# Kernel optimization log

Measured on AMD Instinct MI355X. Metric: run time of the kernel, lower is better.

The kernel has to match this reference:

```python
import jax, jax.numpy as jnp
import numpy as np

T, HID, H, KV, D = 2048, 2048, 16, 8, 128
EPS = 1e-6
THETA = 10000.0


def setup_inputs() -> dict:
    key = jax.random.key(0)
    ks = jax.random.split(key, 6)
    positions = jnp.arange(T, dtype=jnp.int64 if jax.config.jax_enable_x64 else jnp.int32)
    hidden_states = jax.random.normal(ks[0], (T, HID), dtype=jnp.float32)
    scale = 0.02
    Wq = jax.random.normal(ks[1], (HID, H * 2 * D), dtype=jnp.float32) * scale
    Wk = jax.random.normal(ks[2], (HID, KV * D), dtype=jnp.float32) * scale
    Wv = jax.random.normal(ks[3], (HID, KV * D), dtype=jnp.float32) * scale
    Wo = jax.random.normal(ks[4], (H * D, HID), dtype=jnp.float32) * scale
    q_norm_w = jnp.zeros((D,), dtype=jnp.float32)  # torch init: zeros, applied as (1+w)
    k_norm_w = jnp.zeros((D,), dtype=jnp.float32)
    return {"positions": positions, "hidden_states": hidden_states, "Wq": Wq,
            "Wk": Wk, "Wv": Wv, "Wo": Wo, "q_norm_w": q_norm_w, "k_norm_w": k_norm_w}


def _rms_norm(x, w):
    # fp32 RMSNorm with (1 + weight) scaling, per last dim
    xf = x.astype(jnp.float32)
    inv = jax.lax.rsqrt(jnp.mean(xf * xf, axis=-1, keepdims=True) + EPS)
    return (xf * inv * (1.0 + w.astype(jnp.float32))).astype(x.dtype)


def _rope(x, positions):
    # neox-style rotary over full head_dim; x: (T, heads, D)
    half = D // 2
    inv_freq = 1.0 / (THETA ** (jnp.arange(0, half, dtype=jnp.float32) / half))
    freqs = positions.astype(jnp.float32)[:, None] * inv_freq  # (T, half)
    cos = jnp.cos(freqs)[:, None, :]  # (T,1,half)
    sin = jnp.sin(freqs)[:, None, :]
    x1, x2 = x[..., :half], x[..., half:]
    return jnp.concatenate([x1 * cos - x2 * sin, x2 * cos + x1 * sin], axis=-1)


def reference(positions, hidden_states, Wq, Wk, Wv, Wo, q_norm_w, k_norm_w):
    scaling = D ** -0.5
    qg = (hidden_states @ Wq).reshape(T, H, 2 * D)
    q, gate = qg[..., :D], qg[..., D:]              # (T,H,D) each
    k = (hidden_states @ Wk).reshape(T, KV, D)
    v = (hidden_states @ Wv).reshape(T, KV, D)
    q = _rms_norm(q, q_norm_w)
    k = _rms_norm(k, k_norm_w)
    q = _rope(q, positions)
    k = _rope(k, positions)
    # GQA: repeat kv heads
    rep = H // KV
    k = jnp.repeat(k, rep, axis=1)                   # (T,H,D)
    v = jnp.repeat(v, rep, axis=1)
    scores = jnp.einsum('thd,shd->hts', q, k) * scaling  # (H,T,T)
    causal = positions[:, None] >= positions[None, :]     # (T,T)
    scores = jnp.where(causal[None], scores, jnp.finfo(scores.dtype).min)
    probs = jax.nn.softmax(scores, axis=-1)
    o = jnp.einsum('hts,shd->thd', probs, v).reshape(T, H * D)
    o = o * jax.nn.sigmoid(gate.reshape(T, H * D))
    return o @ Wo
```

## Files before the change

kernel.cpp:

```cpp
#include <hip/hip_runtime.h>
#include <stdint.h>
#include <math.h>

#define T_SEQ 2048
#define HID   2048
#define NH    16
#define NKV   8
#define DH    128

typedef __bf16 bf16x8 __attribute__((ext_vector_type(8)));
typedef float  f32x4  __attribute__((ext_vector_type(4)));

__device__ __forceinline__ ushort f2bf(float f) {
  uint32_t u = __float_as_uint(f);
  u += 0x7FFF + ((u >> 16) & 1);
  return (ushort)(u >> 16);
}
__device__ __forceinline__ ushort f2bf_rz(float f) {
  return (ushort)(__float_as_uint(f) >> 16);
}
__device__ __forceinline__ float bf2f(ushort u) {
  return __uint_as_float(((uint32_t)u) << 16);
}
__device__ __forceinline__ void gld16(const void* g, void* l) {
  __builtin_amdgcn_global_load_lds(
      (const __attribute__((address_space(1))) uint32_t*)g,
      (__attribute__((address_space(3))) uint32_t*)l, 16, 0, 0);
}

__global__ __launch_bounds__(256) void prep_kernel(
    const float* __restrict__ hs, const float* __restrict__ Wq,
    const float* __restrict__ Wk, const float* __restrict__ Wv,
    const float* __restrict__ Wo, ushort* __restrict__ hs16,
    ushort* __restrict__ Wqt, ushort* __restrict__ Wkt,
    ushort* __restrict__ Wvt, ushort* __restrict__ Wot) {
  int bid = blockIdx.x;
  if (bid < 4096) {
    int i = (bid * 256 + threadIdx.x) * 4;
    float4 v = *(const float4*)(hs + i);
    ushort4 o = {f2bf(v.x), f2bf(v.y), f2bf(v.z), f2bf(v.w)};
    *(ushort4*)(hs16 + i) = o;
    return;
  }
  bid -= 4096;
  const float* src; ushort* dst; int N, bi, bj;
  if (bid < 2048)      { src = Wq; dst = Wqt; N = 4096; bj = bid & 63; bi = bid >> 6; }
  else if (bid < 2560) { bid -= 2048; src = Wk; dst = Wkt; N = 1024; bj = bid & 15; bi = bid >> 4; }
  else if (bid < 3072) { bid -= 2560; src = Wv; dst = Wvt; N = 1024; bj = bid & 15; bi = bid >> 4; }
  else                 { bid -= 3072; src = Wo; dst = Wot; N = 2048; bj = bid & 31; bi = bid >> 5; }
  __shared__ float tile[64][65];
  const int r = threadIdx.x >> 2, cg = (threadIdx.x & 3) * 16;
  const float* sp = src + (size_t)(bi * 64 + r) * N + bj * 64 + cg;
#pragma unroll
  for (int p = 0; p < 4; ++p) {
    float4 v = *(const float4*)(sp + p * 4);
    tile[r][cg + p * 4 + 0] = v.x; tile[r][cg + p * 4 + 1] = v.y;
    tile[r][cg + p * 4 + 2] = v.z; tile[r][cg + p * 4 + 3] = v.w;
  }
  __syncthreads();
  ushort* dp = dst + (size_t)(bj * 64 + r) * HID + bi * 64 + cg;
#pragma unroll
  for (int p = 0; p < 2; ++p) {
    union { uint4 v; ushort u[8]; } o;
#pragma unroll
    for (int j = 0; j < 8; ++j) o.u[j] = f2bf(tile[cg + p * 8 + j][r]);
    *(uint4*)(dp + p * 8) = o.v;
  }
}

template <int MI>
__device__ __forceinline__ void gemm_loop(
    const ushort* __restrict__ A, const ushort* __restrict__ Bt,
    int K, int m0, int n0, ushort* As, ushort* Bs, f32x4 (*acc)[4]) {
  const int tid = threadIdx.x, lane = tid & 63, w = tid >> 6;
  const int quad = lane >> 4, l15 = lane & 15;
  const int wm = (w >> 1) * (MI * 16), wn = (w & 1) * 64;
  const int srow = tid >> 2, sch = tid & 3;
  for (int k0 = 0; k0 < K; k0 += 32) {
    __syncthreads();
#pragma unroll
    for (int p = 0; p < MI / 2; ++p) {
      int row = p * 64 + srow;
      int gch = sch ^ ((row >> 1) & 3);
      gld16(A + (size_t)(m0 + row) * K + k0 + gch * 8,
            As + (p * 256 + w * 64) * 8);
    }
#pragma unroll
    for (int p = 0; p < 2; ++p) {
      int row = p * 64 + srow;
      int gch = sch ^ ((row >> 1) & 3);
      gld16(Bt + (size_t)(n0 + row) * K + k0 + gch * 8,
            Bs + (p * 256 + w * 64) * 8);
    }
    __syncthreads();
    bf16x8 af[MI], bfr[4];
#pragma unroll
    for (int mi = 0; mi < MI; ++mi) {
      int row = wm + mi * 16 + l15;
      int pch = quad ^ ((row >> 1) & 3);
      af[mi] = *(const bf16x8*)(As + row * 32 + pch * 8);
    }
#pragma unroll
    for (int ni = 0; ni < 4; ++ni) {
      int row = wn + ni * 16 + l15;
      int pch = quad ^ ((row >> 1) & 3);
      bfr[ni] = *(const bf16x8*)(Bs + row * 32 + pch * 8);
    }
#pragma unroll
    for (int mi = 0; mi < MI; ++mi)
#pragma unroll
      for (int ni = 0; ni < 4; ++ni)
        acc[mi][ni] = __builtin_amdgcn_mfma_f32_16x16x32_bf16(
            af[mi], bfr[ni], acc[mi][ni], 0, 0, 0);
  }
}

__device__ __forceinline__ void bf16_store(f32x4 (*acc)[4],
                                           ushort* __restrict__ Cb, int Ncols,
                                           int m0, int n0) {
  const int lane = threadIdx.x & 63, w = threadIdx.x >> 6;
  const int quad = lane >> 4, l15 = lane & 15;
  const int wm = (w >> 1) * 64, wn = (w & 1) * 64;
#pragma unroll
  for (int mi = 0; mi < 4; ++mi)
#pragma unroll
    for (int ni = 0; ni < 4; ++ni)
#pragma unroll
      for (int r = 0; r < 4; ++r) {
        int row = m0 + wm + mi * 16 + quad * 4 + r;
        int col = n0 + wn + ni * 16 + l15;
        Cb[(size_t)row * Ncols + col] = f2bf(acc[mi][ni][r]);
      }
}

__global__ __launch_bounds__(256) void gemm_qkv(
    const ushort* __restrict__ hs16, const ushort* __restrict__ Wqt,
    const ushort* __restrict__ Wkt, const ushort* __restrict__ Wvt,
    ushort* __restrict__ q16, ushort* __restrict__ gate16,
    ushort* __restrict__ k16, ushort* __restrict__ v16t) {
  __shared__ ushort As[128 * 32];
  __shared__ ushort Bs[128 * 32];
  f32x4 acc[4][4];
#pragma unroll
  for (int i = 0; i < 4; ++i)
#pragma unroll
    for (int j = 0; j < 4; ++j) acc[i][j] = (f32x4){0.f, 0.f, 0.f, 0.f};
  const int b = blockIdx.x;
  if (b < 512) {
    int mt = b >> 5, nt = b & 31, m0 = mt * 128;
    gemm_loop<4>(hs16, Wqt, HID, m0, nt * 128, As, Bs, acc);
    ushort* dst = ((nt & 1) == 0) ? q16 : gate16;
    bf16_store(acc, dst, NH * DH, m0, (nt >> 1) * 128);
  } else if (b < 640) {
    int f = b - 512, m0 = (f >> 3) * 128, n0 = (f & 7) * 128;
    gemm_loop<4>(hs16, Wkt, HID, m0, n0, As, Bs, acc);
    bf16_store(acc, k16, 1024, m0, n0);
  } else {
    int f = b - 640, m0 = (f >> 4) * 128, n0 = (f & 15) * 128;
    gemm_loop<4>(Wvt, hs16, HID, m0, n0, As, Bs, acc);
    bf16_store(acc, v16t, T_SEQ, m0, n0);
  }
}

__global__ __launch_bounds__(256) void gemm_out(
    const ushort* __restrict__ ob16, const ushort* __restrict__ Wot,
    float* __restrict__ out) {
  __shared__ ushort As[64 * 32];
  __shared__ ushort Bs[128 * 32];
  f32x4 acc[2][4];
#pragma unroll
  for (int i = 0; i < 2; ++i)
#pragma unroll
    for (int j = 0; j < 4; ++j) acc[i][j] = (f32x4){0.f, 0.f, 0.f, 0.f};
  const int b = blockIdx.x;
  const int m0 = (b >> 4) * 64, n0 = (b & 15) * 128;
  gemm_loop<2>(ob16, Wot, HID, m0, n0, As, Bs, acc);
  const int lane = threadIdx.x & 63, w = threadIdx.x >> 6;
  const int quad = lane >> 4, l15 = lane & 15;
  const int wm = (w >> 1) * 32, wn = (w & 1) * 64;
#pragma unroll
  for (int mi = 0; mi < 2; ++mi)
#pragma unroll
    for (int ni = 0; ni < 4; ++ni)
#pragma unroll
      for (int r = 0; r < 4; ++r) {
        int row = m0 + wm + mi * 16 + quad * 4 + r;
        int col = n0 + wn + ni * 16 + l15;
        out[(size_t)row * HID + col] = acc[mi][ni][r];
      }
}

__global__ __launch_bounds__(128) void norm_qk(
    ushort* __restrict__ q16, ushort* __restrict__ k16,
    const int* __restrict__ positions, const float* __restrict__ qw,
    const float* __restrict__ kw) {
  const int t = blockIdx.x, hh = blockIdx.y, d = threadIdx.x;
  ushort* x; const float* wgt;
  if (hh < NH) { x = q16 + ((size_t)t * NH + hh) * DH; wgt = qw; }
  else         { x = k16 + ((size_t)t * NKV + (hh - NH)) * DH; wgt = kw; }
  float v = bf2f(x[d]);
  float ss = v * v;
#pragma unroll
  for (int off = 32; off >= 1; off >>= 1) ss += __shfl_xor(ss, off, 64);
  __shared__ float red[2];
  if ((d & 63) == 0) red[d >> 6] = ss;
  __syncthreads();
  float mean = (red[0] + red[1]) * (1.0f / 128.0f);
  float xn = v * rsqrtf(mean + 1e-6f) * (1.0f + wgt[d]);
  __shared__ float sh[128];
  sh[d] = xn;
  __syncthreads();
  if (d < 64) {
    float pos = (float)positions[t];
    float rev = pos * exp2f((float)d * -0.20762050593045233f) *
                0.15915494309189535f;
    float fr = rev - floorf(rev);
    float s = __builtin_amdgcn_sinf(fr);
    float c = __builtin_amdgcn_cosf(fr);
    float x1 = sh[d], x2 = sh[d + 64];
    x[d]      = f2bf(x1 * c - x2 * s);
    x[d + 64] = f2bf(x2 * c + x1 * s);
  }
}

__global__ __launch_bounds__(256) void attn_mfma(
    const ushort* __restrict__ q16, const ushort* __restrict__ k16,
    const ushort* __restrict__ v16t, const float* __restrict__ qnw,
    const float* __restrict__ knw, ushort* __restrict__ Op0,
    ushort* __restrict__ Op1, ushort* __restrict__ Op2,
    float* __restrict__ lpart) {
  const int pb = blockIdx.x, h = blockIdx.y, s = blockIdx.z, kvh = h >> 1;
  const int tid = threadIdx.x, lane = tid & 63, w = tid >> 6;
  const int quad = lane >> 4, l15 = lane & 15;

  __shared__ ushort Ks[64 * 128];
  __shared__ ushort Vs[144 * 64];
  __shared__ ushort Ps[4][16][72];

  for (int i = tid; i < 16 * 64; i += 256) {
    int row = 128 + (i >> 6), col = i & 63;
    Vs[row * 64 + col] = (row == 128) ? (ushort)0x3F80 : (ushort)0;
  }

  __shared__ float s8[8];
  __shared__ float bshare;
  {
    float mq = 0.f, mk = 0.f;
    if (tid < 128) { mq = fabsf(1.f + qnw[tid]); mk = fabsf(1.f + knw[tid]); }
#pragma unroll
    for (int off = 32; off >= 1; off >>= 1) {
      mq = fmaxf(mq, __shfl_xor(mq, off, 64));
      mk = fmaxf(mk, __shfl_xor(mk, off, 64));
    }
    if (lane == 0) { s8[w * 2] = mq; s8[w * 2 + 1] = mk; }
    __syncthreads();
    if (tid == 0) {
      float MQ = fmaxf(s8[0], s8[2]), MK = fmaxf(s8[1], s8[3]);
      bshare = 16.3217f * MQ * MK * 1.02f + 0.1f;
    }
    __syncthreads();
  }
  const float B = bshare;
  const float CSC = 0.08838834764831845f * 1.44269504088896f;

#pragma unroll 1
  for (int sel = 0; sel < 2; ++sel) {
    const int qt = sel ? (31 - pb) : pb;
    const int q0 = qt * 64;
    const int ntl = (qt >= s) ? ((qt - s) / 3 + 1) : 0;

    bf16x8 qf[4];
    const ushort* qbase = q16 + ((size_t)(q0 + w * 16 + l15) * NH + h) * DH;
#pragma unroll
    for (int ks = 0; ks < 4; ++ks)
      qf[ks] = *(const bf16x8*)(qbase + ks * 32 + quad * 8);

    f32x4 oacc[9];
#pragma unroll
    for (int i = 0; i < 9; ++i) oacc[i] = (f32x4){0.f, 0.f, 0.f, 0.f};

#pragma unroll 1
    for (int it = 0; it < ntl; ++it) {
      const int kt = s + 3 * it;
      const int kt0 = kt * 64;
      __syncthreads();
#pragma unroll
      for (int p = 0; p < 4; ++p) {
        int row = p * 16 + (tid >> 4), ch = tid & 15;
        int gch = ch ^ (row & 15);
        gld16(k16 + ((size_t)(kt0 + row) * NKV + kvh) * DH + gch * 8,
              Ks + (p * 256 + w * 64) * 8);
      }
#pragma unroll
      for (int p = 0; p < 4; ++p) {
        int row = p * 32 + (tid >> 3), ch = tid & 7;
        int gch = ch ^ (row & 7);
        gld16(v16t + (size_t)(kvh * DH + row) * T_SEQ + kt0 + gch * 8,
              Vs + (p * 256 + w * 64) * 8);
      }
      __syncthreads();

      f32x4 sacc[4];
#pragma unroll
      for (int ni = 0; ni < 4; ++ni) sacc[ni] = (f32x4){0.f, 0.f, 0.f, 0.f};
#pragma unroll
      for (int ks = 0; ks < 4; ++ks)
#pragma unroll
        for (int ni = 0; ni < 4; ++ni) {
          int row = ni * 16 + l15;
          int pch = (ks * 4 + quad) ^ (row & 15);
          bf16x8 kf = *(const bf16x8*)(Ks + row * 128 + pch * 8);
          sacc[ni] = __builtin_amdgcn_mfma_f32_16x16x32_bf16(
              qf[ks], kf, sacc[ni], 0, 0, 0);
        }

      const bool diag = (kt == qt);
#pragma unroll
      for (int ni = 0; ni < 4; ++ni) {
        int key = kt0 + ni * 16 + l15;
#pragma unroll
        for (int r = 0; r < 4; ++r) {
          float arg = fmaf(sacc[ni][r], CSC, -B);
          float pv;
          if (diag) {
            int q = q0 + w * 16 + quad * 4 + r;
            pv = (key <= q) ? exp2f(arg) : 0.f;
          } else {
            pv = exp2f(arg);
          }
          Ps[w][quad * 4 + r][ni * 16 + l15] = f2bf_rz(pv);
        }
      }

#pragma unroll
      for (int ks2 = 0; ks2 < 2; ++ks2) {
        bf16x8 pf = *(const bf16x8*)(&Ps[w][l15][ks2 * 32 + quad * 8]);
#pragma unroll
        for (int ni = 0; ni < 9; ++ni) {
          int row = ni * 16 + l15;
          int pch = (ks2 * 4 + quad) ^ (row & 7);
          bf16x8 vf = *(const bf16x8*)(Vs + row * 64 + pch * 8);
          oacc[ni] = __builtin_amdgcn_mfma_f32_16x16x32_bf16(
              pf, vf, oacc[ni], 0, 0, 0);
        }
      }
    }

    ushort* Op = (s == 0) ? Op0 : (s == 1) ? Op1 : Op2;
#pragma unroll
    for (int ni = 0; ni < 8; ++ni) {
      int d = ni * 16 + l15;
#pragma unroll
      for (int r = 0; r < 4; ++r) {
        int q = q0 + w * 16 + quad * 4 + r;
        Op[((size_t)h * T_SEQ + q) * DH + d] = f2bf(oacc[ni][r]);
      }
    }
    if (l15 == 0) {
#pragma unroll
      for (int r = 0; r < 4; ++r) {
        int q = q0 + w * 16 + quad * 4 + r;
        lpart[(size_t)s * (NH * T_SEQ) + h * T_SEQ + q] = oacc[8][r];
      }
    }
  }
}

__global__ __launch_bounds__(256) void combine_kernel(
    const ushort* __restrict__ Op0, const ushort* __restrict__ Op1,
    const ushort* __restrict__ Op2, const float* __restrict__ lpart,
    const ushort* __restrict__ gate16, ushort* __restrict__ ob16) {
  const int t = blockIdx.x, tid = threadIdx.x;
  const int h = tid >> 4, d0 = (tid & 15) * 8;
  const int NT = NH * T_SEQ;
  const float l = lpart[h * T_SEQ + t] + lpart[NT + h * T_SEQ + t] +
                  lpart[2 * NT + h * T_SEQ + t];
  const float inv = 1.0f / l;
  const size_t po = ((size_t)h * T_SEQ + t) * DH + d0;
  ushort4 a0 = *(const ushort4*)(Op0 + po);
  ushort4 a1 = *(const ushort4*)(Op0 + po + 4);
  ushort4 b0 = *(const ushort4*)(Op1 + po);
  ushort4 b1 = *(const ushort4*)(Op1 + po + 4);
  ushort4 c0 = *(const ushort4*)(Op2 + po);
  ushort4 c1 = *(const ushort4*)(Op2 + po + 4);
  const ushort* gp = gate16 + (size_t)t * (NH * DH) + h * DH + d0;
  ushort4 g0 = *(const ushort4*)(gp);
  ushort4 g1 = *(const ushort4*)(gp + 4);
  float oa[8] = {bf2f(a0.x), bf2f(a0.y), bf2f(a0.z), bf2f(a0.w),
                 bf2f(a1.x), bf2f(a1.y), bf2f(a1.z), bf2f(a1.w)};
  float ob[8] = {bf2f(b0.x), bf2f(b0.y), bf2f(b0.z), bf2f(b0.w),
                 bf2f(b1.x), bf2f(b1.y), bf2f(b1.z), bf2f(b1.w)};
  float oc[8] = {bf2f(c0.x), bf2f(c0.y), bf2f(c0.z), bf2f(c0.w),
                 bf2f(c1.x), bf2f(c1.y), bf2f(c1.z), bf2f(c1.w)};
  float gg[8] = {bf2f(g0.x), bf2f(g0.y), bf2f(g0.z), bf2f(g0.w),
                 bf2f(g1.x), bf2f(g1.y), bf2f(g1.z), bf2f(g1.w)};
  ushort r[8];
#pragma unroll
  for (int i = 0; i < 8; ++i) {
    float o = (oa[i] + ob[i] + oc[i]) * inv;
    o = o / (1.0f + exp2f(-gg[i] * 1.44269504088896f));
    r[i] = f2bf(o);
  }
  ushort* op = ob16 + (size_t)t * (NH * DH) + h * DH + d0;
  *(ushort4*)(op)     = (ushort4){r[0], r[1], r[2], r[3]};
  *(ushort4*)(op + 4) = (ushort4){r[4], r[5], r[6], r[7]};
}

extern "C" void kernel_launch(void* const* d_in, const int* in_sizes, int n_in,
                              void* d_out, int out_size, void* d_ws, size_t ws_size,
                              hipStream_t stream) {
  const int*   positions = (const int*)d_in[0];
  const float* hs  = (const float*)d_in[1];
  const float* Wq  = (const float*)d_in[2];
  const float* Wk  = (const float*)d_in[3];
  const float* Wv  = (const float*)d_in[4];
  const float* Wo  = (const float*)d_in[5];
  const float* qnw = (const float*)d_in[6];
  const float* knw = (const float*)d_in[7];
  float* out = (float*)d_out;

  const size_t MB = 1 << 20;
  uint8_t* ws = (uint8_t*)d_ws;
  ushort* hs16  = (ushort*)(ws + 0);
  ushort* Op0   = (ushort*)(ws + 0);
  ushort* Wqt   = (ushort*)(ws + 8 * MB);
  ushort* Op1   = (ushort*)(ws + 8 * MB);
  ushort* Op2   = (ushort*)(ws + 16 * MB);
  ushort* Wkt   = (ushort*)(ws + 24 * MB);
  ushort* ob16  = (ushort*)(ws + 24 * MB);
  ushort* Wvt   = (ushort*)(ws + 28 * MB);
  ushort* v16t  = (ushort*)(ws + 32 * MB);
  ushort* k16   = (ushort*)(ws + 36 * MB);
  ushort* q16   = (ushort*)(ws + 40 * MB);
  ushort* gate16= (ushort*)(ws + 48 * MB);
  ushort* Wot   = (ushort*)(ws + 56 * MB);
  float*  lpart = (float*)d_out;

  prep_kernel<<<8192, 256, 0, stream>>>(hs, Wq, Wk, Wv, Wo,
                                        hs16, Wqt, Wkt, Wvt, Wot);
  gemm_qkv<<<768, 256, 0, stream>>>(hs16, Wqt, Wkt, Wvt,
                                    q16, gate16, k16, v16t);
  norm_qk<<<dim3(T_SEQ, NH + NKV), 128, 0, stream>>>(q16, k16, positions,
                                                     qnw, knw);
  attn_mfma<<<dim3(16, NH, 3), 256, 0, stream>>>(q16, k16, v16t, qnw, knw,
                                                 Op0, Op1, Op2, lpart);
  combine_kernel<<<T_SEQ, 256, 0, stream>>>(Op0, Op1, Op2, lpart, gate16, ob16);
  gemm_out<<<512, 256, 0, stream>>>(ob16, Wot, out);
}
```

Measured before the change: 281.9 us.

## Replace QKV GEMM with 256x256-tile, 8-wave, pipelined double-buffered kernel

Rewrites the fused QKV projection GEMM to use 256x256 output tiles with 512 threads, a 64-wide K step and double-buffered LDS split into halves. Global loads for the next stages are interleaved with four MFMA phases per K-step, using barriers and s_setprio, to hide memory latency and raise arithmetic intensity. The grid drops from 768 to 192 blocks, which may underfill the device's compute units and lengthen the tail. LDS use grows to 128KB per block, and the epilogue remaps q/gate per head.

```diff
diff --git a/kernel.cpp b/kernel.cpp
--- a/kernel.cpp
+++ b/kernel.cpp
@@ -115,51 +115,166 @@
   }
 }
 
-__device__ __forceinline__ void bf16_store(f32x4 (*acc)[4],
-                                           ushort* __restrict__ Cb, int Ncols,
-                                           int m0, int n0) {
-  const int lane = threadIdx.x & 63, w = threadIdx.x >> 6;
-  const int quad = lane >> 4, l15 = lane & 15;
-  const int wm = (w >> 1) * 64, wn = (w & 1) * 64;
-#pragma unroll
-  for (int mi = 0; mi < 4; ++mi)
-#pragma unroll
-    for (int ni = 0; ni < 4; ++ni)
-#pragma unroll
-      for (int r = 0; r < 4; ++r) {
-        int row = m0 + wm + mi * 16 + quad * 4 + r;
-        int col = n0 + wn + ni * 16 + l15;
-        Cb[(size_t)row * Ncols + col] = f2bf(acc[mi][ni][r]);
-      }
-}
-
-__global__ __launch_bounds__(256) void gemm_qkv(
+
+__device__ __forceinline__ void stage_half(const ushort* __restrict__ X,
+                                           int Ksrc, int rowg0, int k0,
+                                           ushort* lbase) {
+  const int tid = threadIdx.x;
+  const int rl = tid >> 3, ch = tid & 7, w = tid >> 6;
+  const int gch = ch ^ (rl & 7);
+#pragma unroll
+  for (int p = 0; p < 2; ++p)
+    gld16(X + (size_t)(rowg0 + p * 64 + rl) * Ksrc + k0 + gch * 8,
+          lbase + p * 4096 + w * 512);
+}
+
+__device__ __forceinline__ void load_a(const ushort* base, int wr, int quad,
+                                       int l15, bf16x8 af[4][2]) {
+  const int sw = l15 & 7;
+#pragma unroll
+  for (int mi = 0; mi < 4; ++mi) {
+    const ushort* rp = base + (wr * 64 + mi * 16 + l15) * 64;
+#pragma unroll
+    for (int ks = 0; ks < 2; ++ks)
+      af[mi][ks] = *(const bf16x8*)(rp + ((ks * 4 + quad) ^ sw) * 8);
+  }
+}
+__device__ __forceinline__ void load_b(const ushort* base, int wc, int quad,
+                                       int l15, bf16x8 bq[2][2]) {
+  const int sw = l15 & 7;
+#pragma unroll
+  for (int ni = 0; ni < 2; ++ni) {
+    const ushort* rp = base + (wc * 32 + ni * 16 + l15) * 64;
+#pragma unroll
+    for (int ks = 0; ks < 2; ++ks)
+      bq[ni][ks] = *(const bf16x8*)(rp + ((ks * 4 + quad) ^ sw) * 8);
+  }
+}
+__device__ __forceinline__ void mfma_quad(const bf16x8 af[4][2],
+                                          const bf16x8 bq[2][2],
+                                          f32x4 acc[8][4], int mh, int nh) {
+#pragma unroll
+  for (int ks = 0; ks < 2; ++ks)
+#pragma unroll
+    for (int mi = 0; mi < 4; ++mi)
+#pragma unroll
+      for (int ni = 0; ni < 2; ++ni)
+        acc[mh * 4 + mi][nh * 2 + ni] =
+            __builtin_amdgcn_mfma_f32_16x16x32_bf16(
+                af[mi][ks], bq[ni][ks], acc[mh * 4 + mi][nh * 2 + ni], 0, 0, 0);
+}
+
+#define PHASE_MID()                                     \
+  __builtin_amdgcn_s_barrier();                         \
+  asm volatile("s_waitcnt lgkmcnt(0)" ::: "memory");    \
+  __builtin_amdgcn_sched_barrier(0)
+
+__global__ __launch_bounds__(512, 2) void gemm_qkv256(
     const ushort* __restrict__ hs16, const ushort* __restrict__ Wqt,
     const ushort* __restrict__ Wkt, const ushort* __restrict__ Wvt,
     ushort* __restrict__ q16, ushort* __restrict__ gate16,
     ushort* __restrict__ k16, ushort* __restrict__ v16t) {
-  __shared__ ushort As[128 * 32];
-  __shared__ ushort Bs[128 * 32];
-  f32x4 acc[4][4];
-#pragma unroll
-  for (int i = 0; i < 4; ++i)
+  __shared__ ushort As[2][2][8192];
+  __shared__ ushort Bs[2][2][8192];
+
+  const int b = blockIdx.x;
+  const ushort* A; const ushort* Bt; int m0, n0, kind;
+  if (b < 128)      { A = hs16; Bt = Wqt; m0 = (b >> 4) << 8; n0 = (b & 15) << 8; kind = 0; }
+  else if (b < 160) { int f = b - 128; A = hs16; Bt = Wkt; m0 = (f >> 2) << 8; n0 = (f & 3) << 8; kind = 1; }
+  else              { int f = b - 160; A = Wvt; Bt = hs16; m0 = (f >> 3) << 8; n0 = (f & 7) << 8; kind = 2; }
+
+  const int tid = threadIdx.x, lane = tid & 63;
+  const int quad = lane >> 4, l15 = lane & 15;
+  const int wid = tid >> 6, wr = wid >> 2, wc = wid & 3;
+
+  f32x4 acc[8][4];
+#pragma unroll
+  for (int i = 0; i < 8; ++i)
 #pragma unroll
     for (int j = 0; j < 4; ++j) acc[i][j] = (f32x4){0.f, 0.f, 0.f, 0.f};
-  const int b = blockIdx.x;
-  if (b < 512) {
-    int mt = b >> 5, nt = b & 31, m0 = mt * 128;
-    gemm_loop<4>(hs16, Wqt, HID, m0, nt * 128, As, Bs, acc);
-    ushort* dst = ((nt & 1) == 0) ? q16 : gate16;
-    bf16_store(acc, dst, NH * DH, m0, (nt >> 1) * 128);
-  } else if (b < 640) {
-    int f = b - 512, m0 = (f >> 3) * 128, n0 = (f & 7) * 128;
-    gemm_loop<4>(hs16, Wkt, HID, m0, n0, As, Bs, acc);
-    bf16_store(acc, k16, 1024, m0, n0);
-  } else {
-    int f = b - 640, m0 = (f >> 4) * 128, n0 = (f & 15) * 128;
-    gemm_loop<4>(Wvt, hs16, HID, m0, n0, As, Bs, acc);
-    bf16_store(acc, v16t, T_SEQ, m0, n0);
-  }
+
+  constexpr int K = HID;
+  constexpr int NKT = K / 64;
+
+  stage_half(A,  K, m0,        0, &As[0][0][0]);
+  stage_half(A,  K, m0 + 128,  0, &As[0][1][0]);
+  stage_half(Bt, K, n0,        0, &Bs[0][0][0]);
+  stage_half(Bt, K, n0 + 128,  0, &Bs[0][1][0]);
+  stage_half(A,  K, m0,       64, &As[1][0][0]);
+  stage_half(Bt, K, n0 + 128, 64, &Bs[1][1][0]);
+  asm volatile("s_waitcnt vmcnt(4)" ::: "memory");
+  __builtin_amdgcn_s_barrier();
+
+  bf16x8 af[4][2], bq0[2][2], bq1[2][2];
+
+#pragma unroll 1
+  for (int t = 0; t < NKT; ++t) {
+    const int buf = t & 1, nbuf = buf ^ 1;
+    const ushort* pA0 = &As[buf][0][0];
+    const ushort* pA1 = &As[buf][1][0];
+    const ushort* pB0 = &Bs[buf][0][0];
+    const ushort* pB1 = &Bs[buf][1][0];
+    const int kt1 = (t + 1) * 64, kt2 = (t + 2) * 64;
+
+    load_a(pA0, wr, quad, l15, af);
+    load_b(pB0, wc, quad, l15, bq0);
+    if (t + 1 < NKT) stage_half(Bt, K, n0, kt1, &Bs[nbuf][0][0]);
+    PHASE_MID();
+    __builtin_amdgcn_s_setprio(1);
+    mfma_quad(af, bq0, acc, 0, 0);
+    __builtin_amdgcn_s_setprio(0);
+    __builtin_amdgcn_s_barrier();
+
+    load_b(pB1, wc, quad, l15, bq1);
+    if (t + 1 < NKT) stage_half(A, K, m0 + 128, kt1, &As[nbuf][1][0]);
+    PHASE_MID();
+    __builtin_amdgcn_s_setprio(1);
+    mfma_quad(af, bq1, acc, 0, 1);
+    __builtin_amdgcn_s_setprio(0);
+    __builtin_amdgcn_s_barrier();
+
+    load_a(pA1, wr, quad, l15, af);
+    if (t + 2 < NKT) stage_half(A, K, m0, kt2, &As[buf][0][0]);
+    PHASE_MID();
+    __builtin_amdgcn_s_setprio(1);
+    mfma_quad(af, bq1, acc, 1, 1);
+    __builtin_amdgcn_s_setprio(0);
+    __builtin_amdgcn_s_barrier();
+
+    load_b(pB0, wc, quad, l15, bq0);
+    if (t + 2 < NKT) stage_half(Bt, K, n0 + 128, kt2, &Bs[buf][1][0]);
+    PHASE_MID();
+    __builtin_amdgcn_s_setprio(1);
+    mfma_quad(af, bq0, acc, 1, 0);
+    __builtin_amdgcn_s_setprio(0);
+    if (t + 2 < NKT) asm volatile("s_waitcnt vmcnt(4)" ::: "memory");
+    else             asm volatile("s_waitcnt vmcnt(0)" ::: "memory");
+    __builtin_amdgcn_s_barrier();
+  }
+
+  const int head = n0 >> 8;
+#pragma unroll
+  for (int mh = 0; mh < 2; ++mh)
+#pragma unroll
+    for (int mi = 0; mi < 4; ++mi)
+#pragma unroll
+      for (int nh = 0; nh < 2; ++nh)
+#pragma unroll
+        for (int ni = 0; ni < 2; ++ni)
+#pragma unroll
+          for (int r = 0; r < 4; ++r) {
+            const int row = m0 + mh * 128 + wr * 64 + mi * 16 + quad * 4 + r;
+            const int ic = wc * 32 + ni * 16 + l15;
+            const ushort v = f2bf(acc[mh * 4 + mi][nh * 2 + ni][r]);
+            if (kind == 0) {
+              ushort* dst = nh ? gate16 : q16;
+              dst[((size_t)row * NH + head) * DH + ic] = v;
+            } else if (kind == 1) {
+              k16[(size_t)row * 1024 + n0 + nh * 128 + ic] = v;
+            } else {
+              v16t[(size_t)row * T_SEQ + n0 + nh * 128 + ic] = v;
+            }
+          }
 }
 
 __global__ __launch_bounds__(256) void gemm_out(
@@ -438,8 +553,8 @@
 
   prep_kernel<<<8192, 256, 0, stream>>>(hs, Wq, Wk, Wv, Wo,
                                         hs16, Wqt, Wkt, Wvt, Wot);
-  gemm_qkv<<<768, 256, 0, stream>>>(hs16, Wqt, Wkt, Wvt,
-                                    q16, gate16, k16, v16t);
+  gemm_qkv256<<<192, 512, 0, stream>>>(hs16, Wqt, Wkt, Wvt,
+                                       q16, gate16, k16, v16t);
   norm_qk<<<dim3(T_SEQ, NH + NKV), 128, 0, stream>>>(q16, k16, positions,
                                                      qnw, knw);
   attn_mfma<<<dim3(16, NH, 3), 256, 0, stream>>>(q16, k16, v16t, qnw, knw,
```

Measured after the change: 283.7 us. Within noise of the previous version (+0.6%).

## Fuse Q/K RMSNorm and RoPE into the QKV GEMM epilogue

Applied to the files above, without the earlier changes.

Removes the separate norm_qk kernel and applies RMSNorm plus rotary embedding inside the QKV projection epilogue for Q and K tiles. Each 128-column tile is one full head, so the per-row sum of squares is reduced through cross-lane shuffles and shared memory, and the rotated values are written as vectorized 16-byte stores. This avoids a kernel launch and a full read/write round trip of Q and K through global memory. In exchange it needs a larger shared-memory union and extra syncs and transcendental work in the GEMM epilogue, which may raise register pressure.

```diff
diff --git a/kernel.cpp b/kernel.cpp
--- a/kernel.cpp
+++ b/kernel.cpp
@@ -133,13 +133,76 @@
       }
 }
 
+struct SmemQKV {
+  union {
+    struct { ushort As[128 * 32]; ushort Bs[128 * 32]; } g;
+    struct { ushort qn[128][132]; float rss[128][2]; } n;
+  };
+};
+
+__device__ __forceinline__ void norm_rope_store(
+    f32x4 (*acc)[4], ushort* __restrict__ dst, int nheads, int m0, int head,
+    const int* __restrict__ positions, const float* __restrict__ wgt,
+    SmemQKV* sm) {
+  const int tid = threadIdx.x, lane = tid & 63, w = tid >> 6;
+  const int quad = lane >> 4, l15 = lane & 15;
+  const int wm = (w >> 1) * 64, wn = (w & 1) * 64;
+  __syncthreads();
+#pragma unroll
+  for (int mi = 0; mi < 4; ++mi)
+#pragma unroll
+    for (int r = 0; r < 4; ++r) {
+      const int row = wm + mi * 16 + quad * 4 + r;
+      float ss = 0.f;
+#pragma unroll
+      for (int ni = 0; ni < 4; ++ni) {
+        float v = acc[mi][ni][r];
+        ss += v * v;
+        sm->n.qn[row][wn + ni * 16 + l15] = f2bf(v);
+      }
+      ss += __shfl_xor(ss, 8, 64);
+      ss += __shfl_xor(ss, 4, 64);
+      ss += __shfl_xor(ss, 2, 64);
+      ss += __shfl_xor(ss, 1, 64);
+      if (l15 == 0) sm->n.rss[row][w & 1] = ss;
+    }
+  __syncthreads();
+  const int row = tid >> 1, d0 = (tid & 1) * 32;
+  const int t = m0 + row;
+  const float rstd =
+      rsqrtf((sm->n.rss[row][0] + sm->n.rss[row][1]) * (1.f / 128.f) + 1e-6f);
+  const float pos = (float)positions[t];
+  ushort o1[32], o2[32];
+#pragma unroll
+  for (int j = 0; j < 32; ++j) {
+    const int d = d0 + j;
+    float x1 = bf2f(sm->n.qn[row][d]) * rstd * (1.f + wgt[d]);
+    float x2 = bf2f(sm->n.qn[row][d + 64]) * rstd * (1.f + wgt[d + 64]);
+    float rev = pos * exp2f((float)d * -0.20762050593045233f) *
+                0.15915494309189535f;
+    float fr = rev - floorf(rev);
+    float s = __builtin_amdgcn_sinf(fr);
+    float c = __builtin_amdgcn_cosf(fr);
+    o1[j] = f2bf(x1 * c - x2 * s);
+    o2[j] = f2bf(x2 * c + x1 * s);
+  }
+  ushort* op = dst + ((size_t)t * nheads + head) * DH;
+#pragma unroll
+  for (int p = 0; p < 4; ++p)
+    *(uint4*)(op + d0 + p * 8) = *(const uint4*)(o1 + p * 8);
+#pragma unroll
+  for (int p = 0; p < 4; ++p)
+    *(uint4*)(op + 64 + d0 + p * 8) = *(const uint4*)(o2 + p * 8);
+}
+
 __global__ __launch_bounds__(256) void gemm_qkv(
     const ushort* __restrict__ hs16, const ushort* __restrict__ Wqt,
     const ushort* __restrict__ Wkt, const ushort* __restrict__ Wvt,
-    ushort* __restrict__ q16, ushort* __restrict__ gate16,
-    ushort* __restrict__ k16, ushort* __restrict__ v16t) {
-  __shared__ ushort As[128 * 32];
-  __shared__ ushort Bs[128 * 32];
+    const int* __restrict__ positions, const float* __restrict__ qnw,
+    const float* __restrict__ knw, ushort* __restrict__ q16,
+    ushort* __restrict__ gate16, ushort* __restrict__ k16,
+    ushort* __restrict__ v16t) {
+  __shared__ alignas(16) SmemQKV sm;
   f32x4 acc[4][4];
 #pragma unroll
   for (int i = 0; i < 4; ++i)
@@ -148,16 +211,18 @@
   const int b = blockIdx.x;
   if (b < 512) {
     int mt = b >> 5, nt = b & 31, m0 = mt * 128;
-    gemm_loop<4>(hs16, Wqt, HID, m0, nt * 128, As, Bs, acc);
-    ushort* dst = ((nt & 1) == 0) ? q16 : gate16;
-    bf16_store(acc, dst, NH * DH, m0, (nt >> 1) * 128);
+    gemm_loop<4>(hs16, Wqt, HID, m0, nt * 128, sm.g.As, sm.g.Bs, acc);
+    if ((nt & 1) == 0)
+      norm_rope_store(acc, q16, NH, m0, nt >> 1, positions, qnw, &sm);
+    else
+      bf16_store(acc, gate16, NH * DH, m0, (nt >> 1) * 128);
   } else if (b < 640) {
     int f = b - 512, m0 = (f >> 3) * 128, n0 = (f & 7) * 128;
-    gemm_loop<4>(hs16, Wkt, HID, m0, n0, As, Bs, acc);
-    bf16_store(acc, k16, 1024, m0, n0);
+    gemm_loop<4>(hs16, Wkt, HID, m0, n0, sm.g.As, sm.g.Bs, acc);
+    norm_rope_store(acc, k16, NKV, m0, n0 >> 7, positions, knw, &sm);
   } else {
     int f = b - 640, m0 = (f >> 4) * 128, n0 = (f & 15) * 128;
-    gemm_loop<4>(Wvt, hs16, HID, m0, n0, As, Bs, acc);
+    gemm_loop<4>(Wvt, hs16, HID, m0, n0, sm.g.As, sm.g.Bs, acc);
     bf16_store(acc, v16t, T_SEQ, m0, n0);
   }
 }
@@ -188,39 +253,6 @@
         int col = n0 + wn + ni * 16 + l15;
         out[(size_t)row * HID + col] = acc[mi][ni][r];
       }
-}
-
-__global__ __launch_bounds__(128) void norm_qk(
-    ushort* __restrict__ q16, ushort* __restrict__ k16,
-    const int* __restrict__ positions, const float* __restrict__ qw,
-    const float* __restrict__ kw) {
-  const int t = blockIdx.x, hh = blockIdx.y, d = threadIdx.x;
-  ushort* x; const float* wgt;
-  if (hh < NH) { x = q16 + ((size_t)t * NH + hh) * DH; wgt = qw; }
-  else         { x = k16 + ((size_t)t * NKV + (hh - NH)) * DH; wgt = kw; }
-  float v = bf2f(x[d]);
-  float ss = v * v;
-#pragma unroll
-  for (int off = 32; off >= 1; off >>= 1) ss += __shfl_xor(ss, off, 64);
-  __shared__ float red[2];
-  if ((d & 63) == 0) red[d >> 6] = ss;
-  __syncthreads();
-  float mean = (red[0] + red[1]) * (1.0f / 128.0f);
-  float xn = v * rsqrtf(mean + 1e-6f) * (1.0f + wgt[d]);
-  __shared__ float sh[128];
-  sh[d] = xn;
-  __syncthreads();
-  if (d < 64) {
-    float pos = (float)positions[t];
-    float rev = pos * exp2f((float)d * -0.20762050593045233f) *
-                0.15915494309189535f;
-    float fr = rev - floorf(rev);
-    float s = __builtin_amdgcn_sinf(fr);
-    float c = __builtin_amdgcn_cosf(fr);
-    float x1 = sh[d], x2 = sh[d + 64];
-    x[d]      = f2bf(x1 * c - x2 * s);
-    x[d + 64] = f2bf(x2 * c + x1 * s);
-  }
 }
 
 __global__ __launch_bounds__(256) void attn_mfma(
@@ -438,10 +470,8 @@
 
   prep_kernel<<<8192, 256, 0, stream>>>(hs, Wq, Wk, Wv, Wo,
                                         hs16, Wqt, Wkt, Wvt, Wot);
-  gemm_qkv<<<768, 256, 0, stream>>>(hs16, Wqt, Wkt, Wvt,
+  gemm_qkv<<<768, 256, 0, stream>>>(hs16, Wqt, Wkt, Wvt, positions, qnw, knw,
                                     q16, gate16, k16, v16t);
-  norm_qk<<<dim3(T_SEQ, NH + NKV), 128, 0, stream>>>(q16, k16, positions,
-                                                     qnw, knw);
   attn_mfma<<<dim3(16, NH, 3), 256, 0, stream>>>(q16, k16, v16t, qnw, knw,
                                                  Op0, Op1, Op2, lpart);
   combine_kernel<<<T_SEQ, 256, 0, stream>>>(Op0, Op1, Op2, lpart, gate16, ob16);
```

Result: slower. 291.4 us (+3.4%).
